# Optimization experiments

Measured on AMD Instinct MI355X. Metric: run time of the kernel, lower is better.

## Reference

```python
import jax, jax.numpy as jnp
import numpy as np

N_NODES = 50000
N_EDGES = 262144
HID = 256
N_CLS = 2


def setup_inputs() -> dict:
    key = jax.random.key(0)
    ks = jax.random.split(key, 6)
    node_repr = jax.random.normal(ks[0], (N_NODES, HID), dtype=jnp.float32)
    src = jax.random.randint(ks[1], (N_EDGES,), 0, N_NODES, dtype=jnp.int64)
    dst = jax.random.randint(ks[2], (N_EDGES,), 0, N_NODES, dtype=jnp.int64)
    # Linear weights stored as (in, out); init ~ torch default scale
    W1 = jax.random.normal(ks[3], (4 * HID, 2 * HID), dtype=jnp.float32) * (1.0 / np.sqrt(4 * HID))
    b1 = jnp.zeros((2 * HID,), dtype=jnp.float32)
    W2 = jax.random.normal(ks[4], (2 * HID, N_CLS), dtype=jnp.float32) * (1.0 / np.sqrt(2 * HID))
    b2 = jnp.zeros((N_CLS,), dtype=jnp.float32)
    return {"node_repr": node_repr, "src": src, "dst": dst,
            "W1": W1, "b1": b1, "W2": W2, "b2": b2}


def reference(node_repr, src, dst, W1, b1, W2, b2):
    h_i = node_repr[src]                      # [E, H] gather
    h_j = node_repr[dst]                      # [E, H] gather
    edge_input = jnp.concatenate(
        [h_i, h_j, jnp.abs(h_i - h_j), h_i * h_j], axis=1)  # [E, 4H]
    h = jax.nn.relu(edge_input @ W1 + b1)     # [E, 2H]; dropout = identity (eval)
    return h @ W2 + b2                        # [E, C]
```

## Files before the change

kernel.cpp:

```cpp
#include <hip/hip_runtime.h>

#define N_NODES 50000
#define E_EDGES 262144

typedef __attribute__((ext_vector_type(8))) short bf16x8;
typedef __attribute__((ext_vector_type(4))) float f32x4;

union V16 { uint4 u; bf16x8 h; };

__device__ __forceinline__ unsigned rne_pack(float a, float b) {
  unsigned ua = __float_as_uint(a); ua += 0x7fffu + ((ua >> 16) & 1u);
  unsigned ub = __float_as_uint(b); ub += 0x7fffu + ((ub >> 16) & 1u);
  return (ua >> 16) | (ub & 0xffff0000u);
}
__device__ __forceinline__ float bflo(unsigned u) { return __uint_as_float(u << 16); }
__device__ __forceinline__ float bfhi(unsigned u) { return __uint_as_float(u & 0xffff0000u); }
__device__ __forceinline__ unsigned perm_pack(float a, float b) {
  return __builtin_amdgcn_perm(__float_as_uint(b), __float_as_uint(a), 0x07060302u);
}
__device__ __forceinline__ void async_gather16(const void* gptr, void* lptr) {
  __builtin_amdgcn_global_load_lds(
      (const __attribute__((address_space(1))) void*)gptr,
      (__attribute__((address_space(3))) void*)lptr, 16, 0, 0);
}

__global__ void cvt_node_kernel(const float* __restrict__ x, unsigned short* __restrict__ y) {
  int i = (blockIdx.x * 256 + threadIdx.x) * 8;
  float4 f0 = *(const float4*)(x + i);
  float4 f1 = *(const float4*)(x + i + 4);
  uint4 o;
  o.x = rne_pack(f0.x, f0.y);
  o.y = rne_pack(f0.z, f0.w);
  o.z = rne_pack(f1.x, f1.y);
  o.w = rne_pack(f1.z, f1.w);
  *(uint4*)(y + i) = o;
}

__global__ void prep_w1pp2_kernel(const float* __restrict__ w1, unsigned short* __restrict__ w1pp2) {
  int t = blockIdx.x * 256 + threadIdx.x;
  int step = t >> 13;
  int rem = t & 8191;
  int sq = rem >> 9;
  int col = rem & 511;
  int s = sq >> 2, qd = sq & 3;
  int k0 = s * 256 + step * 32 + qd * 8;
  float f[8];
#pragma unroll
  for (int i = 0; i < 8; ++i) f[i] = w1[(size_t)(k0 + i) * 512 + col];
  uint4 o;
  o.x = rne_pack(f[0], f[1]);
  o.y = rne_pack(f[2], f[3]);
  o.z = rne_pack(f[4], f[5]);
  o.w = rne_pack(f[6], f[7]);
  *(uint4*)(w1pp2 + (size_t)t * 8) = o;
}

__global__ void init_out_kernel(float* __restrict__ out, const float* __restrict__ b2) {
  int i = blockIdx.x * 256 + threadIdx.x;
  float2 v; v.x = b2[0]; v.y = b2[1];
  *(float2*)(out + (size_t)i * 2) = v;
}

__global__ __launch_bounds__(256) void edge_mlp_kernel(
    const unsigned short* __restrict__ nodeb,
    const unsigned short* __restrict__ w1pp2,
    const int* __restrict__ src,
    const int* __restrict__ dst,
    const float* __restrict__ b1,
    const float* __restrict__ w2,
    float* __restrict__ out) {
  __shared__ char smem[65536];

  const int tid = threadIdx.x;
  const int wid = tid >> 6;
  const int lane = tid & 63;
  const int quad = lane >> 4;
  const int l16 = lane & 15;
  const int bx = blockIdx.x;
  const int m_idx = ((bx >> 5) << 3) + (bx & 7);
  const int n_idx = (bx >> 3) & 3;
  const int wave_m = wid >> 1;
  const int wave_n = wid & 1;
  const int row0 = m_idx * 128;
  const int wrow0 = row0 + wave_m * 64;
  const int n0 = n_idx * 128 + wave_n * 64;

  const char* nodeB = (const char*)nodeb;
  const char* w1B = (const char*)w1pp2;

  const int eh = tid >> 2;
  const unsigned qsw = (unsigned)(((tid & 3) ^ ((tid >> 3) & 3)) << 4);
  const unsigned oi0 = ((unsigned)src[row0 + eh] << 9) + qsw;
  const unsigned oi1 = ((unsigned)src[row0 + 64 + eh] << 9) + qsw;
  const unsigned oj0 = ((unsigned)dst[row0 + eh] << 9) + qsw;
  const unsigned oj1 = ((unsigned)dst[row0 + 64 + eh] << 9) + qsw;
  const unsigned baset = (unsigned)((n_idx * 128 + (tid & 127)) * 16);
  unsigned bo0[4], bo1[4];
#pragma unroll
  for (int c = 0; c < 4; ++c) {
    unsigned sl = (unsigned)(c >> 1);
    unsigned qd = (unsigned)(((tid >> 7) + 2 * c) & 3);
    bo0[c] = ((sl * 4 + qd) * 8192u) + baset;
    bo1[c] = (((2 + sl) * 4 + qd) * 8192u) + baset;
  }
  const unsigned sdst = (unsigned)(wid * 1024);
  char* Bb0 = smem + 32768;
  char* Bb1 = smem + 49152;

  const unsigned aR = (unsigned)((wave_m * 64 + l16) * 64 + ((quad ^ ((l16 >> 1) & 3)) << 4));
  const unsigned bR = (unsigned)(quad * 2048 + (wave_n * 64 + l16) * 16);

  f32x4 acc[4][4];
#pragma unroll
  for (int mt = 0; mt < 4; ++mt)
#pragma unroll
    for (int nt = 0; nt < 4; ++nt)
      acc[mt][nt] = (f32x4){0.f, 0.f, 0.f, 0.f};

  {
    char* A0 = smem;
    async_gather16(nodeB + oi0, A0 + sdst);
    async_gather16(nodeB + oi1, A0 + 4096 + sdst);
    async_gather16(nodeB + oj0, A0 + 8192 + sdst);
    async_gather16(nodeB + oj1, A0 + 12288 + sdst);
#pragma unroll
    for (int c = 0; c < 4; ++c)
      async_gather16(w1B + bo0[c], Bb0 + c * 4096 + sdst);
  }
  __syncthreads();

  int p = 0;
#pragma unroll 1
  for (int step = 0; step < 8; ++step) {
    const char* Acur = smem + (p << 14);
    const unsigned wstep = (unsigned)step * 131072u;
#pragma unroll
    for (int c = 0; c < 4; ++c)
      async_gather16(w1B + (wstep + bo1[c]), Bb1 + c * 4096 + sdst);

    V16 hi[4], hj[4];
#pragma unroll
    for (int mt = 0; mt < 4; ++mt) {
      hi[mt].u = *(const uint4*)(Acur + aR + mt * 1024);
      hj[mt].u = *(const uint4*)(Acur + 8192 + aR + mt * 1024);
    }
#pragma unroll
    for (int sl = 0; sl < 2; ++sl) {
      V16 bf[4];
#pragma unroll
      for (int nt = 0; nt < 4; ++nt)
        bf[nt].u = *(const uint4*)(Bb0 + sl * 8192 + bR + nt * 256);
#pragma unroll
      for (int mt = 0; mt < 4; ++mt) {
        bf16x8 af = (sl == 0) ? hi[mt].h : hj[mt].h;
#pragma unroll
        for (int nt = 0; nt < 4; ++nt)
          acc[mt][nt] = __builtin_amdgcn_mfma_f32_16x16x32_bf16(af, bf[nt].h, acc[mt][nt], 0, 0, 0);
      }
    }
    __syncthreads();

    if (step < 7) {
      const unsigned aoN = (unsigned)(step + 1) * 64u;
      char* Aalt = smem + ((p ^ 1) << 14);
      async_gather16(nodeB + (oi0 + aoN), Aalt + sdst);
      async_gather16(nodeB + (oi1 + aoN), Aalt + 4096 + sdst);
      async_gather16(nodeB + (oj0 + aoN), Aalt + 8192 + sdst);
      async_gather16(nodeB + (oj1 + aoN), Aalt + 12288 + sdst);
      const unsigned wstepN = wstep + 131072u;
#pragma unroll
      for (int c = 0; c < 4; ++c)
        async_gather16(w1B + (wstepN + bo0[c]), Bb0 + c * 4096 + sdst);
    }
    V16 a2[4], a3[4];
#pragma unroll
    for (int mt = 0; mt < 4; ++mt) {
      const unsigned hw[4] = {hi[mt].u.x, hi[mt].u.y, hi[mt].u.z, hi[mt].u.w};
      const unsigned jw[4] = {hj[mt].u.x, hj[mt].u.y, hj[mt].u.z, hj[mt].u.w};
      unsigned d[4], pr[4];
#pragma unroll
      for (int w = 0; w < 4; ++w) {
        float i0 = bflo(hw[w]), i1 = bfhi(hw[w]);
        float j0 = bflo(jw[w]), j1 = bfhi(jw[w]);
        d[w] = perm_pack(i0 - j0, i1 - j1) & 0x7fff7fffu;
        pr[w] = perm_pack(i0 * j0, i1 * j1);
      }
      a2[mt].u = make_uint4(d[0], d[1], d[2], d[3]);
      a3[mt].u = make_uint4(pr[0], pr[1], pr[2], pr[3]);
    }
#pragma unroll
    for (int sl = 0; sl < 2; ++sl) {
      V16 bf[4];
#pragma unroll
      for (int nt = 0; nt < 4; ++nt)
        bf[nt].u = *(const uint4*)(Bb1 + sl * 8192 + bR + nt * 256);
#pragma unroll
      for (int mt = 0; mt < 4; ++mt) {
        bf16x8 af = (sl == 0) ? a2[mt].h : a3[mt].h;
#pragma unroll
        for (int nt = 0; nt < 4; ++nt)
          acc[mt][nt] = __builtin_amdgcn_mfma_f32_16x16x32_bf16(af, bf[nt].h, acc[mt][nt], 0, 0, 0);
      }
    }
    __syncthreads();
    p ^= 1;
  }

#pragma unroll
  for (int mt = 0; mt < 4; ++mt) {
    float pc0[4] = {0.f, 0.f, 0.f, 0.f};
    float pc1[4] = {0.f, 0.f, 0.f, 0.f};
#pragma unroll
    for (int nt = 0; nt < 4; ++nt) {
      int gc = n0 + nt * 16 + l16;
      float b1v = b1[gc];
      float w20 = w2[gc * 2 + 0];
      float w21 = w2[gc * 2 + 1];
#pragma unroll
      for (int r = 0; r < 4; ++r) {
        float v = fmaxf(acc[mt][nt][r] + b1v, 0.f);
        pc0[r] = fmaf(v, w20, pc0[r]);
        pc1[r] = fmaf(v, w21, pc1[r]);
      }
    }
#pragma unroll
    for (int r = 0; r < 4; ++r) {
      float s0 = pc0[r], s1 = pc1[r];
#pragma unroll
      for (int off = 1; off < 16; off <<= 1) {
        s0 += __shfl_xor(s0, off);
        s1 += __shfl_xor(s1, off);
      }
      int e = wrow0 + mt * 16 + quad * 4 + r;
      if (l16 == 0) unsafeAtomicAdd(&out[(size_t)e * 2 + 0], s0);
      if (l16 == 1) unsafeAtomicAdd(&out[(size_t)e * 2 + 1], s1);
    }
  }
}

extern "C" void kernel_launch(void* const* d_in, const int* in_sizes, int n_in,
                              void* d_out, int out_size, void* d_ws, size_t ws_size,
                              hipStream_t stream) {
  const float* node = (const float*)d_in[0];
  const int* src = (const int*)d_in[1];
  const int* dst = (const int*)d_in[2];
  const float* W1 = (const float*)d_in[3];
  const float* b1 = (const float*)d_in[4];
  const float* W2 = (const float*)d_in[5];
  const float* b2 = (const float*)d_in[6];
  float* out = (float*)d_out;

  unsigned short* nodeb = (unsigned short*)d_ws;
  unsigned short* w1pp2 = (unsigned short*)((char*)d_ws + 25600000);

  cvt_node_kernel<<<6250, 256, 0, stream>>>(node, nodeb);
  prep_w1pp2_kernel<<<256, 256, 0, stream>>>(W1, w1pp2);
  init_out_kernel<<<1024, 256, 0, stream>>>(out, b2);
  edge_mlp_kernel<<<8192, 256, 0, stream>>>(nodeb, w1pp2, src, dst, b1, W2, out);
}
```

Baseline: 484.0 us.

## Load W1 fragments directly from global into registers, halve LDS for occupancy

Staging of the W1 tiles through LDS via async global-to-LDS copies is removed. Each wave now reads its MFMA B fragments straight from global memory (expected to hit L2) into registers. Shared memory drops from 64KB to 32KB, one barrier per step goes away, and launch bounds request two blocks per CU for more occupancy. In exchange, W1 traffic is no longer shared across waves in LDS, so every wave issues redundant global loads. The 16 extra fragment registers per step may also push register pressure against the 2-block occupancy target.

```diff
diff --git a/kernel.cpp b/kernel.cpp
--- a/kernel.cpp
+++ b/kernel.cpp
@@ -61,7 +61,7 @@
   *(float2*)(out + (size_t)i * 2) = v;
 }
 
-__global__ __launch_bounds__(256) void edge_mlp_kernel(
+__global__ __launch_bounds__(256, 2) void edge_mlp_kernel(
     const unsigned short* __restrict__ nodeb,
     const unsigned short* __restrict__ w1pp2,
     const int* __restrict__ src,
@@ -69,7 +69,7 @@
     const float* __restrict__ b1,
     const float* __restrict__ w2,
     float* __restrict__ out) {
-  __shared__ char smem[65536];
+  __shared__ char smem[32768];
 
   const int tid = threadIdx.x;
   const int wid = tid >> 6;
@@ -94,21 +94,14 @@
   const unsigned oi1 = ((unsigned)src[row0 + 64 + eh] << 9) + qsw;
   const unsigned oj0 = ((unsigned)dst[row0 + eh] << 9) + qsw;
   const unsigned oj1 = ((unsigned)dst[row0 + 64 + eh] << 9) + qsw;
-  const unsigned baset = (unsigned)((n_idx * 128 + (tid & 127)) * 16);
-  unsigned bo0[4], bo1[4];
-#pragma unroll
-  for (int c = 0; c < 4; ++c) {
-    unsigned sl = (unsigned)(c >> 1);
-    unsigned qd = (unsigned)(((tid >> 7) + 2 * c) & 3);
-    bo0[c] = ((sl * 4 + qd) * 8192u) + baset;
-    bo1[c] = (((2 + sl) * 4 + qd) * 8192u) + baset;
-  }
   const unsigned sdst = (unsigned)(wid * 1024);
-  char* Bb0 = smem + 32768;
-  char* Bb1 = smem + 49152;
+
+  unsigned bOff[4];
+#pragma unroll
+  for (int s = 0; s < 4; ++s)
+    bOff[s] = (unsigned)((s * 4 + quad) * 8192 + (n0 + l16) * 16);
 
   const unsigned aR = (unsigned)((wave_m * 64 + l16) * 64 + ((quad ^ ((l16 >> 1) & 3)) << 4));
-  const unsigned bR = (unsigned)(quad * 2048 + (wave_n * 64 + l16) * 16);
 
   f32x4 acc[4][4];
 #pragma unroll
@@ -117,49 +110,16 @@
     for (int nt = 0; nt < 4; ++nt)
       acc[mt][nt] = (f32x4){0.f, 0.f, 0.f, 0.f};
 
-  {
-    char* A0 = smem;
-    async_gather16(nodeB + oi0, A0 + sdst);
-    async_gather16(nodeB + oi1, A0 + 4096 + sdst);
-    async_gather16(nodeB + oj0, A0 + 8192 + sdst);
-    async_gather16(nodeB + oj1, A0 + 12288 + sdst);
-#pragma unroll
-    for (int c = 0; c < 4; ++c)
-      async_gather16(w1B + bo0[c], Bb0 + c * 4096 + sdst);
-  }
+  async_gather16(nodeB + oi0, smem + sdst);
+  async_gather16(nodeB + oi1, smem + 4096 + sdst);
+  async_gather16(nodeB + oj0, smem + 8192 + sdst);
+  async_gather16(nodeB + oj1, smem + 12288 + sdst);
   __syncthreads();
 
   int p = 0;
 #pragma unroll 1
   for (int step = 0; step < 8; ++step) {
     const char* Acur = smem + (p << 14);
-    const unsigned wstep = (unsigned)step * 131072u;
-#pragma unroll
-    for (int c = 0; c < 4; ++c)
-      async_gather16(w1B + (wstep + bo1[c]), Bb1 + c * 4096 + sdst);
-
-    V16 hi[4], hj[4];
-#pragma unroll
-    for (int mt = 0; mt < 4; ++mt) {
-      hi[mt].u = *(const uint4*)(Acur + aR + mt * 1024);
-      hj[mt].u = *(const uint4*)(Acur + 8192 + aR + mt * 1024);
-    }
-#pragma unroll
-    for (int sl = 0; sl < 2; ++sl) {
-      V16 bf[4];
-#pragma unroll
-      for (int nt = 0; nt < 4; ++nt)
-        bf[nt].u = *(const uint4*)(Bb0 + sl * 8192 + bR + nt * 256);
-#pragma unroll
-      for (int mt = 0; mt < 4; ++mt) {
-        bf16x8 af = (sl == 0) ? hi[mt].h : hj[mt].h;
-#pragma unroll
-        for (int nt = 0; nt < 4; ++nt)
-          acc[mt][nt] = __builtin_amdgcn_mfma_f32_16x16x32_bf16(af, bf[nt].h, acc[mt][nt], 0, 0, 0);
-      }
-    }
-    __syncthreads();
-
     if (step < 7) {
       const unsigned aoN = (unsigned)(step + 1) * 64u;
       char* Aalt = smem + ((p ^ 1) << 14);
@@ -167,12 +127,30 @@
       async_gather16(nodeB + (oi1 + aoN), Aalt + 4096 + sdst);
       async_gather16(nodeB + (oj0 + aoN), Aalt + 8192 + sdst);
       async_gather16(nodeB + (oj1 + aoN), Aalt + 12288 + sdst);
-      const unsigned wstepN = wstep + 131072u;
-#pragma unroll
-      for (int c = 0; c < 4; ++c)
-        async_gather16(w1B + (wstepN + bo0[c]), Bb0 + c * 4096 + sdst);
-    }
-    V16 a2[4], a3[4];
+    }
+    const unsigned wstep = (unsigned)step * 131072u;
+    V16 bf[4][4];
+#pragma unroll
+    for (int s = 0; s < 4; ++s)
+#pragma unroll
+      for (int nt = 0; nt < 4; ++nt)
+        bf[s][nt].u = *(const uint4*)(w1B + (wstep + bOff[s]) + nt * 256);
+    V16 hi[4], hj[4];
+#pragma unroll
+    for (int mt = 0; mt < 4; ++mt) {
+      hi[mt].u = *(const uint4*)(Acur + aR + mt * 1024);
+      hj[mt].u = *(const uint4*)(Acur + 8192 + aR + mt * 1024);
+    }
+#pragma unroll
+    for (int sl = 0; sl < 2; ++sl) {
+#pragma unroll
+      for (int mt = 0; mt < 4; ++mt) {
+        bf16x8 af = (sl == 0) ? hi[mt].h : hj[mt].h;
+#pragma unroll
+        for (int nt = 0; nt < 4; ++nt)
+          acc[mt][nt] = __builtin_amdgcn_mfma_f32_16x16x32_bf16(af, bf[sl][nt].h, acc[mt][nt], 0, 0, 0);
+      }
+    }
 #pragma unroll
     for (int mt = 0; mt < 4; ++mt) {
       const unsigned hw[4] = {hi[mt].u.x, hi[mt].u.y, hi[mt].u.z, hi[mt].u.w};
@@ -185,22 +163,15 @@
         d[w] = perm_pack(i0 - j0, i1 - j1) & 0x7fff7fffu;
         pr[w] = perm_pack(i0 * j0, i1 * j1);
       }
-      a2[mt].u = make_uint4(d[0], d[1], d[2], d[3]);
-      a3[mt].u = make_uint4(pr[0], pr[1], pr[2], pr[3]);
-    }
-#pragma unroll
-    for (int sl = 0; sl < 2; ++sl) {
-      V16 bf[4];
+      V16 a2, a3;
+      a2.u = make_uint4(d[0], d[1], d[2], d[3]);
+      a3.u = make_uint4(pr[0], pr[1], pr[2], pr[3]);
 #pragma unroll
       for (int nt = 0; nt < 4; ++nt)
-        bf[nt].u = *(const uint4*)(Bb1 + sl * 8192 + bR + nt * 256);
-#pragma unroll
-      for (int mt = 0; mt < 4; ++mt) {
-        bf16x8 af = (sl == 0) ? a2[mt].h : a3[mt].h;
-#pragma unroll
-        for (int nt = 0; nt < 4; ++nt)
-          acc[mt][nt] = __builtin_amdgcn_mfma_f32_16x16x32_bf16(af, bf[nt].h, acc[mt][nt], 0, 0, 0);
-      }
+        acc[mt][nt] = __builtin_amdgcn_mfma_f32_16x16x32_bf16(a2.h, bf[2][nt].h, acc[mt][nt], 0, 0, 0);
+#pragma unroll
+      for (int nt = 0; nt < 4; ++nt)
+        acc[mt][nt] = __builtin_amdgcn_mfma_f32_16x16x32_bf16(a3.h, bf[3][nt].h, acc[mt][nt], 0, 0, 0);
     }
     __syncthreads();
     p ^= 1;
```

Measured after the change: 472.9 us. -2.3%, faster.
